# Kernel tuning notes

Measured on AMD Instinct MI355X. Metric: run time of the kernel, lower is better.

## Reference

```python
import jax, jax.numpy as jnp
import numpy as np

N = 50000
E = 1000000
D_IN = 128
D_HID = 128
D_EMB = 128
D_DEG = 32
NEG_SLOPE = 0.2


def _add_self_loops(src, dst, n):
    loop = jnp.arange(n, dtype=src.dtype)
    return jnp.concatenate([src, loop]), jnp.concatenate([dst, loop])


def gat_conv(x, src, dst, W, a_src, a_dst, b, n):
    """PyG GATConv, heads=1, add_self_loops=True. src/dst already include self loops."""
    h = x @ W                                   # [n, d_out]
    hs = h[src]                                 # [e, d_out] gather (message sources)
    e = jax.nn.leaky_relu(hs @ a_src + h[dst] @ a_dst, NEG_SLOPE)  # [e]
    m = jax.ops.segment_max(e, dst, num_segments=n)
    e = jnp.exp(e - m[dst])
    denom = jax.ops.segment_sum(e, dst, num_segments=n)
    alpha = e / (denom[dst] + 1e-16)
    out = jax.ops.segment_sum(alpha[:, None] * hs, dst, num_segments=n)
    return out + b


def setup_inputs() -> dict:
    key = jax.random.key(0)
    ks = jax.random.split(key, 24)
    p = lambda k, shape: (jax.random.normal(k, shape, dtype=jnp.float32) * 0.05)
    inp = {
        "x_o": jax.random.normal(ks[0], (N, D_IN), dtype=jnp.float32),
        "degree_o": jax.random.normal(ks[1], (N, D_DEG), dtype=jnp.float32),
        "edge_index_o": jax.random.randint(ks[2], (2, E), 0, N, dtype=jnp.int32),
        "edge_index_s": jax.random.randint(ks[3], (2, E), 0, N, dtype=jnp.int32),
        # GAT layer params: o1, o2, s1, s2
        "W_o1": p(ks[4], (D_IN, D_HID)), "a_src_o1": p(ks[5], (D_HID,)), "a_dst_o1": p(ks[6], (D_HID,)), "b_o1": jnp.zeros((D_HID,), jnp.float32),
        "W_o2": p(ks[7], (D_HID, D_EMB)), "a_src_o2": p(ks[8], (D_EMB,)), "a_dst_o2": p(ks[9], (D_EMB,)), "b_o2": jnp.zeros((D_EMB,), jnp.float32),
        "W_s1": p(ks[10], (D_IN, D_HID)), "a_src_s1": p(ks[11], (D_HID,)), "a_dst_s1": p(ks[12], (D_HID,)), "b_s1": jnp.zeros((D_HID,), jnp.float32),
        "W_s2": p(ks[13], (D_HID, D_EMB)), "a_src_s2": p(ks[14], (D_EMB,)), "a_dst_s2": p(ks[15], (D_EMB,)), "b_s2": jnp.zeros((D_EMB,), jnp.float32),
        "W_pred": p(ks[16], (2 * D_EMB + D_DEG, 2)), "b_pred": jnp.zeros((2,), jnp.float32),
    }
    return inp


def reference(x_o, degree_o,
              W_o1, a_src_o1, a_dst_o1, b_o1,
              W_o2, a_src_o2, a_dst_o2, b_o2,
              W_s1, a_src_s1, a_dst_s1, b_s1,
              W_s2, a_src_s2, a_dst_s2, b_s2,
              W_pred, b_pred,
              edge_index_o, edge_index_s):
    n = x_o.shape[0]
    src_o, dst_o = _add_self_loops(edge_index_o[0], edge_index_o[1], n)
    src_s, dst_s = _add_self_loops(edge_index_s[0], edge_index_s[1], n)

    # branch o (original graph); dropout is identity in eval mode
    x1_o = jax.nn.relu(gat_conv(x_o, src_o, dst_o, W_o1, a_src_o1, a_dst_o1, b_o1, n))
    x2_o = gat_conv(x1_o, src_o, dst_o, W_o2, a_src_o2, a_dst_o2, b_o2, n)
    # branch s (second graph)
    x1_s = jax.nn.relu(gat_conv(x_o, src_s, dst_s, W_s1, a_src_s1, a_dst_s1, b_s1, n))
    x2_s = gat_conv(x1_s, src_s, dst_s, W_s2, a_src_s2, a_dst_s2, b_s2, n)

    x2_os = jnp.concatenate([x2_o, x2_s, degree_o], axis=1)   # [n, 2*emb+deg]
    attn = jax.nn.softmax(x2_os @ W_pred + b_pred, axis=1)    # [n, 2]
    pred = attn[:, :1] * x2_o + attn[:, 1:] * x2_s            # [n, emb]
    return pred
```

## Files before the change

kernel.cpp:

```cpp
#include <hip/hip_runtime.h>
#include <hip/hip_fp16.h>
#include <math.h>


#define LRELU(v) ((v) > 0.f ? (v) : 0.2f * (v))

#define BSHIFT 7
#define BSIZE  128
#define MAXB   512
#define CHUNK  4096
#define EPT    16
#define MAXE   4352
#define CAPI   (MAXE + BSIZE)
#define WTSZ   17408

typedef _Float16 half8 __attribute__((ext_vector_type(8)));
typedef float f32x4 __attribute__((ext_vector_type(4)));


__global__ void k_binit(int* bcur_o, int* bcur_s, int nbuck) {
    int i = blockIdx.x * 256 + threadIdx.x;
    if (i < nbuck) { bcur_o[i] = i * MAXE; bcur_s[i] = i * MAXE; }
}

__global__ __launch_bounds__(256) void k_bin_scatter(
    const int* __restrict__ src_o, const int* __restrict__ dst_o,
    const int* __restrict__ src_s, const int* __restrict__ dst_s,
    int* bcur_o, int* bcur_s, int* ebin_o, int* ebin_s, int E)
{
    __shared__ int cnt[MAXB];
    __shared__ int gb[MAXB];
    int t = threadIdx.x;
    int base = blockIdx.x * CHUNK;

    for (int g = 0; g < 2; g++) {
        const int* srcp = g ? src_s : src_o;
        const int* dstp = g ? dst_s : dst_o;
        int* bcur = g ? bcur_s : bcur_o;
        int* ebin = g ? ebin_s : ebin_o;
        for (int i = t; i < MAXB; i += 256) cnt[i] = 0;
        __syncthreads();
        int pk[EPT], bk[EPT], rk[EPT];
        #pragma unroll
        for (int j = 0; j < EPT; j++) {
            int e = base + j * 256 + t;
            bk[j] = -1; pk[j] = 0; rk[j] = 0;
            if (e < E) {
                int d = dstp[e];
                int s = srcp[e];
                int bb = d >> BSHIFT;
                bk[j] = bb;
                pk[j] = ((d & (BSIZE - 1)) << 16) | s;
                rk[j] = atomicAdd(&cnt[bb], 1);
            }
        }
        __syncthreads();
        for (int i = t; i < MAXB; i += 256) {
            int c = cnt[i];
            gb[i] = c ? atomicAdd(&bcur[i], c) : 0;
        }
        __syncthreads();
        #pragma unroll
        for (int j = 0; j < EPT; j++) {
            if (bk[j] >= 0) {
                int p = gb[bk[j]] + rk[j];
                if (p < (bk[j] + 1) * MAXE) ebin[p] = pk[j];
            }
        }
        __syncthreads();
    }
}

__global__ __launch_bounds__(256) void k_sort(
    const int* __restrict__ ebin_o, const int* __restrict__ bcur_o,
    int* __restrict__ off_o, int* __restrict__ dend_o, unsigned short* __restrict__ idx_o,
    const int* __restrict__ ebin_s, const int* __restrict__ bcur_s,
    int* __restrict__ off_s, int* __restrict__ dend_s, unsigned short* __restrict__ idx_s,
    int N)
{
    const int* ebin = blockIdx.y ? ebin_s : ebin_o;
    const int* bcur = blockIdx.y ? bcur_s : bcur_o;
    int* off  = blockIdx.y ? off_s  : off_o;
    int* dend = blockIdx.y ? dend_s : dend_o;
    unsigned short* idx = blockIdx.y ? idx_s : idx_o;

    __shared__ int pack[MAXE];
    __shared__ int sorted[MAXE + BSIZE];
    __shared__ int cnt[BSIZE + 1];
    __shared__ int s2[BSIZE + 1];
    __shared__ int noff[BSIZE + 1];

    int b = blockIdx.x;
    int t = threadIdx.x;
    int node0 = b << BSHIFT;
    int nloc = min(BSIZE, N - node0);
    int ebeg = b * MAXE;
    int ne = min(bcur[b] - ebeg, MAXE);
    int ib = b * CAPI;

    for (int i = t; i < ne; i += 256) pack[i] = ebin[ebeg + i];
    if (t < BSIZE + 1) cnt[t] = (t < nloc) ? 1 : 0;
    __syncthreads();
    for (int i = t; i < ne; i += 256) atomicAdd(&cnt[pack[i] >> 16], 1);
    __syncthreads();
    if (t < BSIZE + 1) s2[t] = cnt[t];
    __syncthreads();
    for (int d = 1; d <= BSIZE; d <<= 1) {
        int v = (t < BSIZE + 1 && t >= d) ? s2[t - d] : 0;
        __syncthreads();
        if (t < BSIZE + 1) s2[t] += v;
        __syncthreads();
    }
    if (t < BSIZE + 1) noff[t] = s2[t] - cnt[t];
    __syncthreads();
    if (t < nloc) {
        off[node0 + t]  = ib + noff[t];
        dend[node0 + t] = ib + s2[t];
        cnt[t] = noff[t] + 1;
        sorted[noff[t]] = node0 + t;
    }
    __syncthreads();
    for (int i = t; i < ne; i += 256) {
        int p = atomicAdd(&cnt[pack[i] >> 16], 1);
        sorted[p] = pack[i] & 0xffff;
    }
    __syncthreads();
    int tot = ne + nloc;
    for (int i = t; i < tot; i += 256) idx[ib + i] = (unsigned short)sorted[i];
}


__global__ __launch_bounds__(256) void k_prepw(
    const float* __restrict__ W0, const float* __restrict__ W1,
    const float* __restrict__ W2, const float* __restrict__ W3,
    _Float16* __restrict__ WtG)
{
    int i = blockIdx.x * 256 + threadIdx.x;
    int w = i >> 14;
    int rem = i & 16383;
    int nn = rem >> 7;
    int k = rem & 127;
    const float* W = (w == 0) ? W0 : (w == 1) ? W1 : (w == 2) ? W2 : W3;
    WtG[w * WTSZ + nn * 136 + k] = (_Float16)W[k * 128 + nn];
}


template<typename IT>
__global__ __launch_bounds__(256) void k_gemm2(
    const IT* __restrict__ X0, const IT* __restrict__ X1,
    const _Float16* __restrict__ WtA, const _Float16* __restrict__ WtB,
    const float* __restrict__ as0, const float* __restrict__ ad0,
    const float* __restrict__ as1, const float* __restrict__ ad1,
    __half* __restrict__ H0, __half* __restrict__ H1,
    float* __restrict__ S0, float* __restrict__ D0,
    float* __restrict__ S1, float* __restrict__ D1,
    int n)
{
    int br = blockIdx.y;
    const IT* X = br ? X1 : X0;
    const _Float16* WtGp = br ? WtB : WtA;
    const float* a_src = br ? as1 : as0;
    const float* a_dst = br ? ad1 : ad0;
    __half* H = br ? H1 : H0;
    float* Svec = br ? S1 : S0;
    float* Dvec = br ? D1 : D0;

    __shared__ _Float16 As[64 * 136];
    __shared__ _Float16 Wt[128 * 136];
    int tid = threadIdx.x;
    int m0 = blockIdx.x * 64;

    for (int i = tid; i < WTSZ / 8; i += 256)
        ((uint4*)Wt)[i] = ((const uint4*)WtGp)[i];
    if constexpr (sizeof(IT) == 4) {
        for (int i = tid; i < 64 * 32; i += 256) {
            int r = i >> 5;
            int c4 = (i & 31) << 2;
            int row = m0 + r; if (row >= n) row = n - 1;
            float4 v = *(const float4*)&X[(size_t)row * 128 + c4];
            _Float16* p = &As[r * 136 + c4];
            p[0] = (_Float16)v.x; p[1] = (_Float16)v.y;
            p[2] = (_Float16)v.z; p[3] = (_Float16)v.w;
        }
    } else {
        for (int i = tid; i < 64 * 16; i += 256) {
            int r = i >> 4;
            int c8 = (i & 15) << 3;
            int row = m0 + r; if (row >= n) row = n - 1;
            *(uint4*)&As[r * 136 + c8] =
                *(const uint4*)&X[(size_t)row * 128 + c8];
        }
    }
    __syncthreads();

    int wave = tid >> 6;
    int lane = tid & 63;
    int m = lane & 15;
    int q = lane >> 4;
    int arow = wave * 16 + m;

    f32x4 acc[8];
    #pragma unroll
    for (int nt = 0; nt < 8; nt++) acc[nt] = (f32x4){0.f, 0.f, 0.f, 0.f};

    #pragma unroll
    for (int k0 = 0; k0 < 128; k0 += 32) {
        half8 a = *(half8*)&As[arow * 136 + k0 + q * 8];
        #pragma unroll
        for (int nt = 0; nt < 8; nt++) {
            half8 b = *(half8*)&Wt[(nt * 16 + m) * 136 + k0 + q * 8];
            acc[nt] = __builtin_amdgcn_mfma_f32_16x16x32_f16(a, b, acc[nt], 0, 0, 0);
        }
    }

    float sp[4] = {0.f, 0.f, 0.f, 0.f};
    float dp[4] = {0.f, 0.f, 0.f, 0.f};
    #pragma unroll
    for (int nt = 0; nt < 8; nt++) {
        float asv = a_src[nt * 16 + m];
        float adv = a_dst[nt * 16 + m];
        #pragma unroll
        for (int r = 0; r < 4; r++) {
            sp[r] = fmaf(acc[nt][r], asv, sp[r]);
            dp[r] = fmaf(acc[nt][r], adv, dp[r]);
        }
    }
    #pragma unroll
    for (int msk = 1; msk < 16; msk <<= 1) {
        #pragma unroll
        for (int r = 0; r < 4; r++) {
            sp[r] += __shfl_xor(sp[r], msk);
            dp[r] += __shfl_xor(dp[r], msk);
        }
    }
    if (m == 0) {
        #pragma unroll
        for (int r = 0; r < 4; r++) {
            int row = m0 + wave * 16 + q * 4 + r;
            if (row < n) { Svec[row] = sp[r]; Dvec[row] = dp[r]; }
        }
    }

    #pragma unroll
    for (int nt = 0; nt < 8; nt++) {
        #pragma unroll
        for (int r = 0; r < 4; r++) {
            As[(wave * 16 + q * 4 + r) * 136 + nt * 16 + m] = (_Float16)acc[nt][r];
        }
    }
    __syncthreads();
    for (int i = tid; i < 1024; i += 256) {
        int r = i >> 4;
        int c8 = (i & 15) << 3;
        int row = m0 + r;
        if (row < n)
            *(uint4*)&H[(size_t)row * 128 + c8] = *(uint4*)&As[r * 136 + c8];
    }
}


__device__ __forceinline__ void agg_core(
    const __half* __restrict__ H, const float* __restrict__ Svec, float dn,
    const unsigned short* __restrict__ idx, int beg, int end,
    int lane, int q, int subl, float* acc, float& denom)
{
    #pragma unroll
    for (int j = 0; j < 8; j++) acc[j] = 0.f;
    denom = 0.f;
    for (int base = beg; base < end; base += 64) {
        int cnt = min(64, end - base);
        int pk = 0;
        if (lane < cnt) {
            int s = idx[base + lane];
            float v = Svec[s] + dn;
            float w = __expf(LRELU(v));
            _Float16 wh = (_Float16)w;
            denom += (float)wh;
            pk = ((int)__builtin_bit_cast(unsigned short, wh) << 16) | s;
        }
        int cnt16 = (cnt + 15) & ~15;
        for (int kk = 0; kk < cnt16; kk += 16) {
            int k0 = kk + q;
            int p0 = __shfl(pk, k0);
            int p1 = __shfl(pk, k0 + 4);
            int p2 = __shfl(pk, k0 + 8);
            int p3 = __shfl(pk, k0 + 12);
            uint4 u0 = ((const uint4*)(H + (size_t)(p0 & 0xffff) * 128))[subl];
            uint4 u1 = ((const uint4*)(H + (size_t)(p1 & 0xffff) * 128))[subl];
            uint4 u2 = ((const uint4*)(H + (size_t)(p2 & 0xffff) * 128))[subl];
            uint4 u3 = ((const uint4*)(H + (size_t)(p3 & 0xffff) * 128))[subl];
            float w0 = (float)__builtin_bit_cast(_Float16, (unsigned short)(p0 >> 16));
            float w1 = (float)__builtin_bit_cast(_Float16, (unsigned short)(p1 >> 16));
            float w2 = (float)__builtin_bit_cast(_Float16, (unsigned short)(p2 >> 16));
            float w3 = (float)__builtin_bit_cast(_Float16, (unsigned short)(p3 >> 16));
            const _Float16* p;
            p = (const _Float16*)&u0;
            #pragma unroll
            for (int j = 0; j < 8; j++) acc[j] = fmaf((float)p[j], w0, acc[j]);
            p = (const _Float16*)&u1;
            #pragma unroll
            for (int j = 0; j < 8; j++) acc[j] = fmaf((float)p[j], w1, acc[j]);
            p = (const _Float16*)&u2;
            #pragma unroll
            for (int j = 0; j < 8; j++) acc[j] = fmaf((float)p[j], w2, acc[j]);
            p = (const _Float16*)&u3;
            #pragma unroll
            for (int j = 0; j < 8; j++) acc[j] = fmaf((float)p[j], w3, acc[j]);
        }
    }
    #pragma unroll
    for (int j = 0; j < 8; j++) {
        acc[j] += __shfl_xor(acc[j], 16);
        acc[j] += __shfl_xor(acc[j], 32);
    }
    #pragma unroll
    for (int o = 32; o; o >>= 1) denom += __shfl_xor(denom, o);
}


__global__ __launch_bounds__(256) void k_agg1(
    const __half* __restrict__ H0, const __half* __restrict__ H1,
    const float* __restrict__ S0, const float* __restrict__ D0,
    const float* __restrict__ S1, const float* __restrict__ D1,
    const int* __restrict__ off0, const int* __restrict__ dend0,
    const unsigned short* __restrict__ idx0,
    const int* __restrict__ off1, const int* __restrict__ dend1,
    const unsigned short* __restrict__ idx1,
    const float* __restrict__ b0, const float* __restrict__ b1,
    __half* __restrict__ out0, __half* __restrict__ out1,
    int n)
{
    int br = blockIdx.y;
    const __half* H = br ? H1 : H0;
    const float* Svec = br ? S1 : S0;
    const float* Dvec = br ? D1 : D0;
    const int* off  = br ? off1  : off0;
    const int* dend = br ? dend1 : dend0;
    const unsigned short* idx = br ? idx1 : idx0;
    const float* bias = br ? b1 : b0;
    __half* out = br ? out1 : out0;

    int wave = threadIdx.x >> 6;
    int lane = threadIdx.x & 63;
    int node = blockIdx.x * 4 + wave;
    if (node >= n) return;

    int q = lane >> 4;
    int subl = lane & 15;
    float acc[8], denom;
    agg_core(H, Svec, Dvec[node], idx, off[node], dend[node],
             lane, q, subl, acc, denom);

    if (q == 0) {
        float inv = 1.f / (denom + 1e-16f);
        int cb = subl << 3;
        half8 hv;
        #pragma unroll
        for (int j = 0; j < 8; j++) {
            float v = fmaxf(acc[j] * inv + bias[cb + j], 0.f);
            hv[j] = (_Float16)v;
        }
        *(half8*)&out[(size_t)node * 128 + cb] = hv;
    }
}


__global__ __launch_bounds__(256) void k_agg_pred(
    const __half* __restrict__ H0, const __half* __restrict__ H1,
    const float* __restrict__ S0, const float* __restrict__ D0,
    const float* __restrict__ S1, const float* __restrict__ D1,
    const int* __restrict__ off0, const int* __restrict__ dend0,
    const unsigned short* __restrict__ idx0,
    const int* __restrict__ off1, const int* __restrict__ dend1,
    const unsigned short* __restrict__ idx1,
    const float* __restrict__ b0, const float* __restrict__ b1,
    const float* __restrict__ deg,
    const float* __restrict__ Wp, const float* __restrict__ bp,
    float* __restrict__ out, int n)
{
    int wave = threadIdx.x >> 6;
    int lane = threadIdx.x & 63;
    int node = blockIdx.x * 4 + wave;
    if (node >= n) return;

    int q = lane >> 4;
    int subl = lane & 15;
    int cb = subl << 3;

    float acc[8], denom;
    float vo[8], vs[8];

    agg_core(H0, S0, D0[node], idx0, off0[node], dend0[node],
             lane, q, subl, acc, denom);
    {
        float inv = 1.f / (denom + 1e-16f);
        #pragma unroll
        for (int j = 0; j < 8; j++) vo[j] = acc[j] * inv + b0[cb + j];
    }
    agg_core(H1, S1, D1[node], idx1, off1[node], dend1[node],
             lane, q, subl, acc, denom);
    {
        float inv = 1.f / (denom + 1e-16f);
        #pragma unroll
        for (int j = 0; j < 8; j++) vs[j] = acc[j] * inv + b1[cb + j];
    }

    if (q == 0) {
        float z0 = 0.f, z1 = 0.f;
        #pragma unroll
        for (int j = 0; j < 8; j++) {
            int c = cb + j;
            z0 = fmaf(vo[j], Wp[c * 2],     z0);
            z1 = fmaf(vo[j], Wp[c * 2 + 1], z1);
            z0 = fmaf(vs[j], Wp[(128 + c) * 2],     z0);
            z1 = fmaf(vs[j], Wp[(128 + c) * 2 + 1], z1);
        }
        float2 dv = *(const float2*)&deg[(size_t)node * 32 + 2 * subl];
        z0 = fmaf(dv.x, Wp[(256 + 2 * subl) * 2],     z0);
        z1 = fmaf(dv.x, Wp[(256 + 2 * subl) * 2 + 1], z1);
        z0 = fmaf(dv.y, Wp[(257 + 2 * subl) * 2],     z0);
        z1 = fmaf(dv.y, Wp[(257 + 2 * subl) * 2 + 1], z1);
        #pragma unroll
        for (int msk = 1; msk < 16; msk <<= 1) {
            z0 += __shfl_xor(z0, msk);
            z1 += __shfl_xor(z1, msk);
        }
        z0 += bp[0];
        z1 += bp[1];
        float mz = fmaxf(z0, z1);
        float e0 = __expf(z0 - mz);
        float e1 = __expf(z1 - mz);
        float a0 = e0 / (e0 + e1);
        float a1 = 1.f - a0;
        float4 r0, r1;
        r0.x = a0 * vo[0] + a1 * vs[0];
        r0.y = a0 * vo[1] + a1 * vs[1];
        r0.z = a0 * vo[2] + a1 * vs[2];
        r0.w = a0 * vo[3] + a1 * vs[3];
        r1.x = a0 * vo[4] + a1 * vs[4];
        r1.y = a0 * vo[5] + a1 * vs[5];
        r1.z = a0 * vo[6] + a1 * vs[6];
        r1.w = a0 * vo[7] + a1 * vs[7];
        *(float4*)&out[(size_t)node * 128 + cb] = r0;
        *(float4*)&out[(size_t)node * 128 + cb + 4] = r1;
    }
}


extern "C" void kernel_launch(void* const* d_in, const int* in_sizes, int n_in,
                              void* d_out, int out_size, void* d_ws, size_t ws_size,
                              hipStream_t stream) {
    const float* x_o    = (const float*)d_in[0];
    const float* degree = (const float*)d_in[1];
    const int*   ei_o   = (const int*)d_in[2];
    const int*   ei_s   = (const int*)d_in[3];
    const float* W_o1 = (const float*)d_in[4];
    const float* asr_o1 = (const float*)d_in[5];
    const float* ads_o1 = (const float*)d_in[6];
    const float* b_o1 = (const float*)d_in[7];
    const float* W_o2 = (const float*)d_in[8];
    const float* asr_o2 = (const float*)d_in[9];
    const float* ads_o2 = (const float*)d_in[10];
    const float* b_o2 = (const float*)d_in[11];
    const float* W_s1 = (const float*)d_in[12];
    const float* asr_s1 = (const float*)d_in[13];
    const float* ads_s1 = (const float*)d_in[14];
    const float* b_s1 = (const float*)d_in[15];
    const float* W_s2 = (const float*)d_in[16];
    const float* asr_s2 = (const float*)d_in[17];
    const float* ads_s2 = (const float*)d_in[18];
    const float* b_s2 = (const float*)d_in[19];
    const float* W_pred = (const float*)d_in[20];
    const float* b_pred = (const float*)d_in[21];
    float* out = (float*)d_out;

    const int N = in_sizes[0] / 128;
    const int E = in_sizes[2] / 2;
    const int NBUCK = (N + BSIZE - 1) >> BSHIFT;

    char* ws = (char*)d_ws;
    size_t o = 0;
    auto alloc = [&](size_t bytes) -> char* {
        char* p = ws + o;
        o += (bytes + 255) & ~(size_t)255;
        return p;
    };
    int* bcur_o = (int*)alloc((size_t)NBUCK * 4);
    int* bcur_s = (int*)alloc((size_t)NBUCK * 4);
    int* off_o  = (int*)alloc((size_t)N * 4);
    int* dend_o = (int*)alloc((size_t)N * 4);
    int* off_s  = (int*)alloc((size_t)N * 4);
    int* dend_s = (int*)alloc((size_t)N * 4);
    unsigned short* idx_o = (unsigned short*)alloc((size_t)NBUCK * CAPI * 2);
    unsigned short* idx_s = (unsigned short*)alloc((size_t)NBUCK * CAPI * 2);
    _Float16* WtG = (_Float16*)alloc((size_t)4 * WTSZ * 2);
    float* Sv_o = (float*)alloc((size_t)N * 4);
    float* Dv_o = (float*)alloc((size_t)N * 4);
    float* Sv_s = (float*)alloc((size_t)N * 4);
    float* Dv_s = (float*)alloc((size_t)N * 4);
    __half* h_o   = (__half*)alloc((size_t)N * 128 * 2);
    __half* h_s   = (__half*)alloc((size_t)N * 128 * 2);
    __half* x1h_o = (__half*)alloc((size_t)N * 128 * 2);
    __half* x1h_s = (__half*)alloc((size_t)N * 128 * 2);
    (void)ws_size;

    int* ebin_o = (int*)h_o;
    int* ebin_s = (int*)h_s;

    dim3 blk(256);
    int gBin  = (E + CHUNK - 1) / CHUNK;
    int gGemm = (N + 63) / 64;
    int gNode = (N + 3) / 4;

    k_binit<<<(NBUCK + 255) / 256, blk, 0, stream>>>(bcur_o, bcur_s, NBUCK);
    k_prepw<<<256, blk, 0, stream>>>(W_o1, W_o2, W_s1, W_s2, WtG);
    k_bin_scatter<<<gBin, blk, 0, stream>>>(ei_o, ei_o + E, ei_s, ei_s + E,
                                            bcur_o, bcur_s, ebin_o, ebin_s, E);
    dim3 gSort(NBUCK, 2);
    k_sort<<<gSort, blk, 0, stream>>>(ebin_o, bcur_o, off_o, dend_o, idx_o,
                                      ebin_s, bcur_s, off_s, dend_s, idx_s, N);

    dim3 gG(gGemm, 2), gA(gNode, 2);
    k_gemm2<float><<<gG, blk, 0, stream>>>(
        x_o, x_o, WtG, WtG + 2 * WTSZ,
        asr_o1, ads_o1, asr_s1, ads_s1,
        h_o, h_s, Sv_o, Dv_o, Sv_s, Dv_s, N);
    k_agg1<<<gA, blk, 0, stream>>>(
        h_o, h_s, Sv_o, Dv_o, Sv_s, Dv_s,
        off_o, dend_o, idx_o, off_s, dend_s, idx_s,
        b_o1, b_s1, x1h_o, x1h_s, N);
    k_gemm2<__half><<<gG, blk, 0, stream>>>(
        x1h_o, x1h_s, WtG + WTSZ, WtG + 3 * WTSZ,
        asr_o2, ads_o2, asr_s2, ads_s2,
        h_o, h_s, Sv_o, Dv_o, Sv_s, Dv_s, N);
    k_agg_pred<<<gNode, blk, 0, stream>>>(
        h_o, h_s, Sv_o, Dv_o, Sv_s, Dv_s,
        off_o, dend_o, idx_o, off_s, dend_s, idx_s,
        b_o2, b_s2, degree, W_pred, b_pred, out, N);
}
```

Baseline: 364.2 us.

## Fuse first-layer GEMMs, per-wave sort histograms, and drop binit launch

The first-layer GEMM becomes a single kernel that loads and converts each x tile once and multiplies it by both branch weight matrices, instead of launching two branch blocks that each read x. The sort kernel gives each wave its own histogram, so shared-memory atomic contention drops. The bucket-cursor init is folded into the weight-prep kernel, removing one launch. The aggregation loop now shuffles fp32 weights and indices separately instead of packing an fp16 weight into the index word, which costs more shuffles but keeps the weights in full precision.

```diff
diff --git a/kernel.cpp b/kernel.cpp
--- a/kernel.cpp
+++ b/kernel.cpp
@@ -17,11 +17,6 @@
 typedef _Float16 half8 __attribute__((ext_vector_type(8)));
 typedef float f32x4 __attribute__((ext_vector_type(4)));
 
-
-__global__ void k_binit(int* bcur_o, int* bcur_s, int nbuck) {
-    int i = blockIdx.x * 256 + threadIdx.x;
-    if (i < nbuck) { bcur_o[i] = i * MAXE; bcur_s[i] = i * MAXE; }
-}
 
 __global__ __launch_bounds__(256) void k_bin_scatter(
     const int* __restrict__ src_o, const int* __restrict__ dst_o,
@@ -86,12 +81,13 @@
 
     __shared__ int pack[MAXE];
     __shared__ int sorted[MAXE + BSIZE];
-    __shared__ int cnt[BSIZE + 1];
+    __shared__ int cnt4[4][BSIZE + 1];
     __shared__ int s2[BSIZE + 1];
     __shared__ int noff[BSIZE + 1];
 
     int b = blockIdx.x;
     int t = threadIdx.x;
+    int wave = t >> 6;
     int node0 = b << BSHIFT;
     int nloc = min(BSIZE, N - node0);
     int ebeg = b * MAXE;
@@ -99,11 +95,16 @@
     int ib = b * CAPI;
 
     for (int i = t; i < ne; i += 256) pack[i] = ebin[ebeg + i];
-    if (t < BSIZE + 1) cnt[t] = (t < nloc) ? 1 : 0;
-    __syncthreads();
-    for (int i = t; i < ne; i += 256) atomicAdd(&cnt[pack[i] >> 16], 1);
-    __syncthreads();
-    if (t < BSIZE + 1) s2[t] = cnt[t];
+    for (int i = t; i < 4 * (BSIZE + 1); i += 256) ((int*)cnt4)[i] = 0;
+    __syncthreads();
+    for (int i = t; i < ne; i += 256) atomicAdd(&cnt4[wave][pack[i] >> 16], 1);
+    __syncthreads();
+    int c0 = 0, c1 = 0, c2 = 0, c3 = 0, selfc = 0;
+    if (t < BSIZE + 1) {
+        c0 = cnt4[0][t]; c1 = cnt4[1][t]; c2 = cnt4[2][t]; c3 = cnt4[3][t];
+        selfc = (t < nloc) ? 1 : 0;
+        s2[t] = c0 + c1 + c2 + c3 + selfc;
+    }
     __syncthreads();
     for (int d = 1; d <= BSIZE; d <<= 1) {
         int v = (t < BSIZE + 1 && t >= d) ? s2[t - d] : 0;
@@ -111,17 +112,21 @@
         if (t < BSIZE + 1) s2[t] += v;
         __syncthreads();
     }
-    if (t < BSIZE + 1) noff[t] = s2[t] - cnt[t];
+    if (t < BSIZE + 1) noff[t] = s2[t] - (c0 + c1 + c2 + c3 + selfc);
     __syncthreads();
     if (t < nloc) {
+        int base0 = noff[t] + 1;
+        cnt4[0][t] = base0;
+        cnt4[1][t] = base0 + c0;
+        cnt4[2][t] = base0 + c0 + c1;
+        cnt4[3][t] = base0 + c0 + c1 + c2;
+        sorted[noff[t]] = node0 + t;
         off[node0 + t]  = ib + noff[t];
         dend[node0 + t] = ib + s2[t];
-        cnt[t] = noff[t] + 1;
-        sorted[noff[t]] = node0 + t;
     }
     __syncthreads();
     for (int i = t; i < ne; i += 256) {
-        int p = atomicAdd(&cnt[pack[i] >> 16], 1);
+        int p = atomicAdd(&cnt4[wave][pack[i] >> 16], 1);
         sorted[p] = pack[i] & 0xffff;
     }
     __syncthreads();
@@ -133,9 +138,10 @@
 __global__ __launch_bounds__(256) void k_prepw(
     const float* __restrict__ W0, const float* __restrict__ W1,
     const float* __restrict__ W2, const float* __restrict__ W3,
-    _Float16* __restrict__ WtG)
+    _Float16* __restrict__ WtG, int* bcur_o, int* bcur_s, int nbuck)
 {
     int i = blockIdx.x * 256 + threadIdx.x;
+    if (i < nbuck) { bcur_o[i] = i * MAXE; bcur_s[i] = i * MAXE; }
     int w = i >> 14;
     int rem = i & 16383;
     int nn = rem >> 7;
@@ -145,9 +151,140 @@
 }
 
 
-template<typename IT>
+__device__ __forceinline__ void sd_epilogue(
+    const f32x4* acc, const float* a_src, const float* a_dst,
+    float* Svec, float* Dvec, int m0, int wave, int lane, int m, int q, int n)
+{
+    float sp[4] = {0.f, 0.f, 0.f, 0.f};
+    float dp[4] = {0.f, 0.f, 0.f, 0.f};
+    #pragma unroll
+    for (int nt = 0; nt < 8; nt++) {
+        float asv = a_src[nt * 16 + m];
+        float adv = a_dst[nt * 16 + m];
+        #pragma unroll
+        for (int r = 0; r < 4; r++) {
+            sp[r] = fmaf(acc[nt][r], asv, sp[r]);
+            dp[r] = fmaf(acc[nt][r], adv, dp[r]);
+        }
+    }
+    #pragma unroll
+    for (int msk = 1; msk < 16; msk <<= 1) {
+        #pragma unroll
+        for (int r = 0; r < 4; r++) {
+            sp[r] += __shfl_xor(sp[r], msk);
+            dp[r] += __shfl_xor(dp[r], msk);
+        }
+    }
+    if (m == 0) {
+        #pragma unroll
+        for (int r = 0; r < 4; r++) {
+            int row = m0 + wave * 16 + q * 4 + r;
+            if (row < n) { Svec[row] = sp[r]; Dvec[row] = dp[r]; }
+        }
+    }
+}
+
+__device__ __forceinline__ void d_to_lds(
+    _Float16* As, const f32x4* acc, int wave, int m, int q)
+{
+    #pragma unroll
+    for (int nt = 0; nt < 8; nt++) {
+        #pragma unroll
+        for (int r = 0; r < 4; r++) {
+            As[(wave * 16 + q * 4 + r) * 136 + nt * 16 + m] = (_Float16)acc[nt][r];
+        }
+    }
+}
+
+__device__ __forceinline__ void lds_to_h(
+    const _Float16* As, __half* H, int m0, int tid, int n)
+{
+    for (int i = tid; i < 1024; i += 256) {
+        int r = i >> 4;
+        int c8 = (i & 15) << 3;
+        int row = m0 + r;
+        if (row < n)
+            *(uint4*)&H[(size_t)row * 128 + c8] = *(const uint4*)&As[r * 136 + c8];
+    }
+}
+
+
+__global__ __launch_bounds__(256, 4) void k_gemm1(
+    const float* __restrict__ X,
+    const _Float16* __restrict__ WtO, const _Float16* __restrict__ WtS,
+    const float* __restrict__ asO, const float* __restrict__ adO,
+    const float* __restrict__ asS, const float* __restrict__ adS,
+    __half* __restrict__ HO, __half* __restrict__ HS,
+    float* __restrict__ SO, float* __restrict__ DO,
+    float* __restrict__ SS, float* __restrict__ DS, int n)
+{
+    __shared__ _Float16 As[64 * 136];
+    __shared__ _Float16 Wt[128 * 136];
+    int tid = threadIdx.x;
+    int m0 = blockIdx.x * 64;
+
+    for (int i = tid; i < WTSZ / 8; i += 256)
+        ((uint4*)Wt)[i] = ((const uint4*)WtO)[i];
+    for (int i = tid; i < 64 * 32; i += 256) {
+        int r = i >> 5;
+        int c4 = (i & 31) << 2;
+        int row = m0 + r; if (row >= n) row = n - 1;
+        float4 v = *(const float4*)&X[(size_t)row * 128 + c4];
+        _Float16* p = &As[r * 136 + c4];
+        p[0] = (_Float16)v.x; p[1] = (_Float16)v.y;
+        p[2] = (_Float16)v.z; p[3] = (_Float16)v.w;
+    }
+    __syncthreads();
+
+    int wave = tid >> 6;
+    int lane = tid & 63;
+    int m = lane & 15;
+    int q = lane >> 4;
+    int arow = wave * 16 + m;
+
+    f32x4 accO[8], accS[8];
+    #pragma unroll
+    for (int nt = 0; nt < 8; nt++) accO[nt] = (f32x4){0.f, 0.f, 0.f, 0.f};
+    #pragma unroll
+    for (int k0 = 0; k0 < 128; k0 += 32) {
+        half8 a = *(half8*)&As[arow * 136 + k0 + q * 8];
+        #pragma unroll
+        for (int nt = 0; nt < 8; nt++) {
+            half8 b = *(half8*)&Wt[(nt * 16 + m) * 136 + k0 + q * 8];
+            accO[nt] = __builtin_amdgcn_mfma_f32_16x16x32_f16(a, b, accO[nt], 0, 0, 0);
+        }
+    }
+    sd_epilogue(accO, asO, adO, SO, DO, m0, wave, lane, m, q, n);
+    __syncthreads();
+    for (int i = tid; i < WTSZ / 8; i += 256)
+        ((uint4*)Wt)[i] = ((const uint4*)WtS)[i];
+    __syncthreads();
+    #pragma unroll
+    for (int nt = 0; nt < 8; nt++) accS[nt] = (f32x4){0.f, 0.f, 0.f, 0.f};
+    #pragma unroll
+    for (int k0 = 0; k0 < 128; k0 += 32) {
+        half8 a = *(half8*)&As[arow * 136 + k0 + q * 8];
+        #pragma unroll
+        for (int nt = 0; nt < 8; nt++) {
+            half8 b = *(half8*)&Wt[(nt * 16 + m) * 136 + k0 + q * 8];
+            accS[nt] = __builtin_amdgcn_mfma_f32_16x16x32_f16(a, b, accS[nt], 0, 0, 0);
+        }
+    }
+    sd_epilogue(accS, asS, adS, SS, DS, m0, wave, lane, m, q, n);
+
+    __syncthreads();
+    d_to_lds(As, accO, wave, m, q);
+    __syncthreads();
+    lds_to_h(As, HO, m0, tid, n);
+    __syncthreads();
+    d_to_lds(As, accS, wave, m, q);
+    __syncthreads();
+    lds_to_h(As, HS, m0, tid, n);
+}
+
+
 __global__ __launch_bounds__(256) void k_gemm2(
-    const IT* __restrict__ X0, const IT* __restrict__ X1,
+    const __half* __restrict__ X0, const __half* __restrict__ X1,
     const _Float16* __restrict__ WtA, const _Float16* __restrict__ WtB,
     const float* __restrict__ as0, const float* __restrict__ ad0,
     const float* __restrict__ as1, const float* __restrict__ ad1,
@@ -157,7 +294,7 @@
     int n)
 {
     int br = blockIdx.y;
-    const IT* X = br ? X1 : X0;
+    const __half* X = br ? X1 : X0;
     const _Float16* WtGp = br ? WtB : WtA;
     const float* a_src = br ? as1 : as0;
     const float* a_dst = br ? ad1 : ad0;
@@ -172,24 +309,11 @@
 
     for (int i = tid; i < WTSZ / 8; i += 256)
         ((uint4*)Wt)[i] = ((const uint4*)WtGp)[i];
-    if constexpr (sizeof(IT) == 4) {
-        for (int i = tid; i < 64 * 32; i += 256) {
-            int r = i >> 5;
-            int c4 = (i & 31) << 2;
-            int row = m0 + r; if (row >= n) row = n - 1;
-            float4 v = *(const float4*)&X[(size_t)row * 128 + c4];
-            _Float16* p = &As[r * 136 + c4];
-            p[0] = (_Float16)v.x; p[1] = (_Float16)v.y;
-            p[2] = (_Float16)v.z; p[3] = (_Float16)v.w;
-        }
-    } else {
-        for (int i = tid; i < 64 * 16; i += 256) {
-            int r = i >> 4;
-            int c8 = (i & 15) << 3;
-            int row = m0 + r; if (row >= n) row = n - 1;
-            *(uint4*)&As[r * 136 + c8] =
-                *(const uint4*)&X[(size_t)row * 128 + c8];
-        }
+    for (int i = tid; i < 64 * 16; i += 256) {
+        int r = i >> 4;
+        int c8 = (i & 15) << 3;
+        int row = m0 + r; if (row >= n) row = n - 1;
+        *(uint4*)&As[r * 136 + c8] = *(const uint4*)&X[(size_t)row * 128 + c8];
     }
     __syncthreads();
 
@@ -202,7 +326,6 @@
     f32x4 acc[8];
     #pragma unroll
     for (int nt = 0; nt < 8; nt++) acc[nt] = (f32x4){0.f, 0.f, 0.f, 0.f};
-
     #pragma unroll
     for (int k0 = 0; k0 < 128; k0 += 32) {
         half8 a = *(half8*)&As[arow * 136 + k0 + q * 8];
@@ -212,50 +335,11 @@
             acc[nt] = __builtin_amdgcn_mfma_f32_16x16x32_f16(a, b, acc[nt], 0, 0, 0);
         }
     }
-
-    float sp[4] = {0.f, 0.f, 0.f, 0.f};
-    float dp[4] = {0.f, 0.f, 0.f, 0.f};
-    #pragma unroll
-    for (int nt = 0; nt < 8; nt++) {
-        float asv = a_src[nt * 16 + m];
-        float adv = a_dst[nt * 16 + m];
-        #pragma unroll
-        for (int r = 0; r < 4; r++) {
-            sp[r] = fmaf(acc[nt][r], asv, sp[r]);
-            dp[r] = fmaf(acc[nt][r], adv, dp[r]);
-        }
-    }
-    #pragma unroll
-    for (int msk = 1; msk < 16; msk <<= 1) {
-        #pragma unroll
-        for (int r = 0; r < 4; r++) {
-            sp[r] += __shfl_xor(sp[r], msk);
-            dp[r] += __shfl_xor(dp[r], msk);
-        }
-    }
-    if (m == 0) {
-        #pragma unroll
-        for (int r = 0; r < 4; r++) {
-            int row = m0 + wave * 16 + q * 4 + r;
-            if (row < n) { Svec[row] = sp[r]; Dvec[row] = dp[r]; }
-        }
-    }
-
-    #pragma unroll
-    for (int nt = 0; nt < 8; nt++) {
-        #pragma unroll
-        for (int r = 0; r < 4; r++) {
-            As[(wave * 16 + q * 4 + r) * 136 + nt * 16 + m] = (_Float16)acc[nt][r];
-        }
-    }
-    __syncthreads();
-    for (int i = tid; i < 1024; i += 256) {
-        int r = i >> 4;
-        int c8 = (i & 15) << 3;
-        int row = m0 + r;
-        if (row < n)
-            *(uint4*)&H[(size_t)row * 128 + c8] = *(uint4*)&As[r * 136 + c8];
-    }
+    sd_epilogue(acc, a_src, a_dst, Svec, Dvec, m0, wave, lane, m, q, n);
+    __syncthreads();
+    d_to_lds(As, acc, wave, m, q);
+    __syncthreads();
+    lds_to_h(As, H, m0, tid, n);
 }
 
 
@@ -269,30 +353,28 @@
     denom = 0.f;
     for (int base = beg; base < end; base += 64) {
         int cnt = min(64, end - base);
-        int pk = 0;
+        float w = 0.f;
+        int s = 0;
         if (lane < cnt) {
-            int s = idx[base + lane];
-            float v = Svec[s] + dn;
-            float w = __expf(LRELU(v));
-            _Float16 wh = (_Float16)w;
-            denom += (float)wh;
-            pk = ((int)__builtin_bit_cast(unsigned short, wh) << 16) | s;
-        }
+            s = idx[base + lane];
+            w = __expf(LRELU(Svec[s] + dn));
+        }
+        denom += w;
         int cnt16 = (cnt + 15) & ~15;
         for (int kk = 0; kk < cnt16; kk += 16) {
             int k0 = kk + q;
-            int p0 = __shfl(pk, k0);
-            int p1 = __shfl(pk, k0 + 4);
-            int p2 = __shfl(pk, k0 + 8);
-            int p3 = __shfl(pk, k0 + 12);
-            uint4 u0 = ((const uint4*)(H + (size_t)(p0 & 0xffff) * 128))[subl];
-            uint4 u1 = ((const uint4*)(H + (size_t)(p1 & 0xffff) * 128))[subl];
-            uint4 u2 = ((const uint4*)(H + (size_t)(p2 & 0xffff) * 128))[subl];
-            uint4 u3 = ((const uint4*)(H + (size_t)(p3 & 0xffff) * 128))[subl];
-            float w0 = (float)__builtin_bit_cast(_Float16, (unsigned short)(p0 >> 16));
-            float w1 = (float)__builtin_bit_cast(_Float16, (unsigned short)(p1 >> 16));
-            float w2 = (float)__builtin_bit_cast(_Float16, (unsigned short)(p2 >> 16));
-            float w3 = (float)__builtin_bit_cast(_Float16, (unsigned short)(p3 >> 16));
+            float w0 = __shfl(w, k0);
+            float w1 = __shfl(w, k0 + 4);
+            float w2 = __shfl(w, k0 + 8);
+            float w3 = __shfl(w, k0 + 12);
+            int s0 = __shfl(s, k0);
+            int s1 = __shfl(s, k0 + 4);
+            int s2 = __shfl(s, k0 + 8);
+            int s3 = __shfl(s, k0 + 12);
+            uint4 u0 = ((const uint4*)(H + (size_t)s0 * 128))[subl];
+            uint4 u1 = ((const uint4*)(H + (size_t)s1 * 128))[subl];
+            uint4 u2 = ((const uint4*)(H + (size_t)s2 * 128))[subl];
+            uint4 u3 = ((const uint4*)(H + (size_t)s3 * 128))[subl];
             const _Float16* p;
             p = (const _Float16*)&u0;
             #pragma unroll
@@ -512,24 +594,25 @@
     int gGemm = (N + 63) / 64;
     int gNode = (N + 3) / 4;
 
-    k_binit<<<(NBUCK + 255) / 256, blk, 0, stream>>>(bcur_o, bcur_s, NBUCK);
-    k_prepw<<<256, blk, 0, stream>>>(W_o1, W_o2, W_s1, W_s2, WtG);
+    k_prepw<<<256, blk, 0, stream>>>(W_o1, W_o2, W_s1, W_s2, WtG,
+                                     bcur_o, bcur_s, NBUCK);
     k_bin_scatter<<<gBin, blk, 0, stream>>>(ei_o, ei_o + E, ei_s, ei_s + E,
                                             bcur_o, bcur_s, ebin_o, ebin_s, E);
     dim3 gSort(NBUCK, 2);
     k_sort<<<gSort, blk, 0, stream>>>(ebin_o, bcur_o, off_o, dend_o, idx_o,
                                       ebin_s, bcur_s, off_s, dend_s, idx_s, N);
 
-    dim3 gG(gGemm, 2), gA(gNode, 2);
-    k_gemm2<float><<<gG, blk, 0, stream>>>(
-        x_o, x_o, WtG, WtG + 2 * WTSZ,
+    k_gemm1<<<gGemm, blk, 0, stream>>>(
+        x_o, WtG, WtG + 2 * WTSZ,
         asr_o1, ads_o1, asr_s1, ads_s1,
         h_o, h_s, Sv_o, Dv_o, Sv_s, Dv_s, N);
+    dim3 gA(gNode, 2);
     k_agg1<<<gA, blk, 0, stream>>>(
         h_o, h_s, Sv_o, Dv_o, Sv_s, Dv_s,
         off_o, dend_o, idx_o, off_s, dend_s, idx_s,
         b_o1, b_s1, x1h_o, x1h_s, N);
-    k_gemm2<__half><<<gG, blk, 0, stream>>>(
+    dim3 gG(gGemm, 2);
+    k_gemm2<<<gG, blk, 0, stream>>>(
         x1h_o, x1h_s, WtG + WTSZ, WtG + 3 * WTSZ,
         asr_o2, ads_o2, asr_s2, ads_s2,
         h_o, h_s, Sv_o, Dv_o, Sv_s, Dv_s, N);
```

New measurement: 353.5 us. 2.9% less time.
